# Performance work log

Measured on AMD Instinct MI355X. Metric: run time of the kernel, lower is better.

## Reference

```python
import jax, jax.numpy as jnp
import numpy as np

PATCH = 16       # patch_size
HALF = 8         # patch_size // 2
SEARCH_HALF = 20 # search_size // 2
NCAND = 40       # candidates per axis (stride=1)
WIN = NCAND + PATCH  # 56: search window side
NUM_PATCHES = 256
IMG_RES = 256    # hard-coded in `patch_ids * H // 256`
EPS = 1e-7


def setup_inputs() -> dict:
    key = jax.random.key(0)
    k0, k1, k2, k3, k4 = jax.random.split(key, 5)
    feat0 = jax.random.normal(k0, (1, 3, 256, 256), jnp.float32)
    feat1 = jax.random.normal(k1, (1, 256, 256, 256), jnp.float32)
    feat2 = jax.random.normal(k2, (1, 512, 128, 128), jnp.float32)
    feat3 = jax.random.normal(k3, (1, 1024, 64, 64), jnp.float32)
    # interior location so the 40x40 candidate grid is full (static shape)
    sample_loc = jax.random.randint(k4, (2,), 28, 228, dtype=jnp.int32)
    return {"feat0": feat0, "feat1": feat1, "feat2": feat2,
            "feat3": feat3, "sample_loc": sample_loc}


def _l2norm(x):
    # Normalize(power=2): x / (sqrt(sum(x^2, dim=1)) + 1e-7)
    norm = jnp.sqrt(jnp.sum(x * x, axis=1, keepdims=True))
    return x / (norm + EPS)


def _select_patch_ids(img, sample_loc):
    # brute-force SSD search of 16x16 patches in a 40x40 stride-1 grid
    C = img.shape[1]
    lh, lw = sample_loc[0], sample_loc[1]
    window = jax.lax.dynamic_slice(
        img, (0, 0, lh - SEARCH_HALF - HALF, lw - SEARCH_HALF - HALF),
        (1, C, WIN, WIN))[0]                       # [C,56,56]
    idx = jnp.arange(NCAND)[:, None] + jnp.arange(PATCH)[None, :]  # [40,16]
    # all candidate patches: [C,40,40,16,16]
    patches = window[:, idx[:, None, :, None], idx[None, :, None, :]]
    sample = jax.lax.dynamic_slice(
        img, (0, 0, lh - HALF, lw - HALF), (1, C, PATCH, PATCH))[0]  # [C,16,16]
    diff = patches - sample[:, None, None, :, :]
    dist = jnp.sqrt(jnp.sum(diff * diff, axis=(0, 3, 4)))  # [40,40] L2 distance
    # topk smallest, sorted ascending
    _, top_idx = jax.lax.top_k(-dist.reshape(-1), NUM_PATCHES)
    hs = lh - SEARCH_HALF + jnp.arange(NCAND)
    ws = lw - SEARCH_HALF + jnp.arange(NCAND)
    locs = jnp.stack(jnp.meshgrid(hs, ws, indexing='ij'), axis=-1).reshape(-1, 2)
    return locs[top_idx].astype(jnp.int32)  # [256,2]


def _gather_norm(feat, patch_ids):
    B, C, H, W = feat.shape
    feat_reshape = feat.transpose(0, 2, 3, 1).reshape(B, H * W, C)
    feat_patch_loc = (patch_ids * H) // IMG_RES          # floor_divide
    patch_id = feat_patch_loc[:, 0] * W + feat_patch_loc[:, 1]
    x_sample = feat_reshape[:, patch_id, :].reshape(-1, C)  # [B*256, C]
    return _l2norm(x_sample)


def reference(feat0, feat1, feat2, feat3, sample_loc):
    patch_ids = _select_patch_ids(feat0, sample_loc)
    outs = tuple(_gather_norm(f, patch_ids) for f in (feat0, feat1, feat2, feat3))
    return (*outs, patch_ids)
```

## Files before the change

kernel.cpp:

```cpp
#include <hip/hip_runtime.h>

#define NCAND 40
#define NC2   1600
#define NP    256

__global__ void k_dist(const float* __restrict__ feat0,
                       const int* __restrict__ loc,
                       float* __restrict__ dist) {
    __shared__ float smp[3 * 16 * 16];
    const int lh = loc[0], lw = loc[1];
    for (int t = threadIdx.x; t < 768; t += 256) {
        int c = t >> 8;
        int rem = t & 255;
        int a = rem >> 4;
        int b = rem & 15;
        smp[t] = feat0[c * 65536 + (lh - 8 + a) * 256 + (lw - 8 + b)];
    }
    __syncthreads();

    const int wid  = threadIdx.x >> 6;
    const int lane = threadIdx.x & 63;
    const int cand = blockIdx.x * 4 + wid;
    const int i = cand / NCAND;
    const int j = cand % NCAND;
    const int base_h = lh - 28 + i;
    const int base_w = lw - 28 + j;

    int c = lane >> 4;
    if (c > 2) c = 0;
    const int h = (lane >> 3) & 1;
    const int u = lane & 7;
    const float* fp = feat0 + c * 65536;
    const float* sc = smp + c * 256;

    float r = 0.0f;
#pragma unroll
    for (int k = 0; k < 16; ++k) {
        const int idx = h * 128 + k * 8 + u;
        const int a = idx >> 4;
        const int b = idx & 15;
        float v = fp[(base_h + a) * 256 + base_w + b];
        float d = __fsub_rn(v, sc[idx]);
        float sq = __fmul_rn(d, d);
        r = (k == 0) ? sq : __fadd_rn(r, sq);
    }
    r = __fadd_rn(r, __shfl_xor(r, 1, 64));
    r = __fadd_rn(r, __shfl_xor(r, 2, 64));
    r = __fadd_rn(r, __shfl_xor(r, 4, 64));
    r = __fadd_rn(r, __shfl_xor(r, 8, 64));
    float p1 = __shfl(r, 16, 64);
    float p2 = __shfl(r, 32, 64);
    float tot = __fadd_rn(__fadd_rn(r, p1), p2);
    if (lane == 0) dist[cand] = __fsqrt_rn(tot);
}

__global__ void k_rank(const float* __restrict__ dist,
                       const int* __restrict__ loc,
                       int* __restrict__ hw,
                       float* __restrict__ out_ids) {
    __shared__ float ds[NC2];
    for (int k = threadIdx.x; k < NC2; k += 256) ds[k] = dist[k];
    __syncthreads();

    const int wid  = threadIdx.x >> 6;
    const int lane = threadIdx.x & 63;
    const int t = blockIdx.x * 4 + wid;
    const float dt = ds[t];
    int rank = 0;
#pragma unroll
    for (int m = 0; m < NC2 / 64; ++m) {
        const int k = lane + (m << 6);
        const float dk = ds[k];
        rank += (dk < dt || (dk == dt && k < t)) ? 1 : 0;
    }
    rank += __shfl_xor(rank, 1, 64);
    rank += __shfl_xor(rank, 2, 64);
    rank += __shfl_xor(rank, 4, 64);
    rank += __shfl_xor(rank, 8, 64);
    rank += __shfl_xor(rank, 16, 64);
    rank += __shfl_xor(rank, 32, 64);

    if (lane == 0 && rank < NP) {
        const int lh = loc[0], lw = loc[1];
        const int h = lh - 20 + t / NCAND;
        const int w = lw - 20 + t % NCAND;
        hw[rank * 2]     = h;
        hw[rank * 2 + 1] = w;
        out_ids[rank * 2]     = (float)h;
        out_ids[rank * 2 + 1] = (float)w;
    }
}

__global__ void k_gather(const float* __restrict__ f0,
                         const float* __restrict__ f1,
                         const float* __restrict__ f2,
                         const float* __restrict__ f3,
                         const int* __restrict__ hw,
                         float* __restrict__ out) {
    const int r = blockIdx.x & 255;
    const int f = blockIdx.x >> 8;

    const float* src;
    int C, H;
    long off;
    if (f == 0)      { src = f0; C = 3;    H = 256; off = 0; }
    else if (f == 1) { src = f1; C = 256;  H = 256; off = 768; }
    else if (f == 2) { src = f2; C = 512;  H = 128; off = 768 + 65536; }
    else             { src = f3; C = 1024; H = 64;  off = 768 + 65536 + 131072; }
    const int W = H;

    const int h = hw[r * 2], w = hw[r * 2 + 1];
    const int hh = (h * H) / 256;
    const int ww = (w * H) / 256;
    const long base = (long)hh * W + ww;
    const long HW = (long)H * W;

    float x[4];
    double acc = 0.0;
    int n = 0;
    for (int c = threadIdx.x; c < C; c += 256) {
        float v = src[(long)c * HW + base];
        x[n++] = v;
        acc = fma((double)v, (double)v, acc);
    }

    for (int o = 32; o > 0; o >>= 1) acc += __shfl_down(acc, o, 64);
    __shared__ double red[4];
    const int lane = threadIdx.x & 63;
    const int wid  = threadIdx.x >> 6;
    if (lane == 0) red[wid] = acc;
    __syncthreads();
    const double total = red[0] + red[1] + red[2] + red[3];
    const float scale = (float)(1.0 / (sqrt(total) + 1e-7));

    n = 0;
    for (int c = threadIdx.x; c < C; c += 256) {
        out[off + (long)r * C + c] = x[n++] * scale;
    }
}

extern "C" void kernel_launch(void* const* d_in, const int* in_sizes, int n_in,
                              void* d_out, int out_size, void* d_ws, size_t ws_size,
                              hipStream_t stream) {
    const float* feat0 = (const float*)d_in[0];
    const float* feat1 = (const float*)d_in[1];
    const float* feat2 = (const float*)d_in[2];
    const float* feat3 = (const float*)d_in[3];
    const int*   loc   = (const int*)d_in[4];
    float* out = (float*)d_out;

    float* dist = (float*)d_ws;
    int* hw = (int*)((char*)d_ws + NC2 * sizeof(float));

    float* out_ids = out + 768 + 65536 + 131072 + 262144;

    k_dist<<<NC2 / 4, 256, 0, stream>>>(feat0, loc, dist);
    k_rank<<<NC2 / 4, 256, 0, stream>>>(dist, loc, hw, out_ids);
    k_gather<<<4 * NP, 256, 0, stream>>>(feat0, feat1, feat2, feat3, hw, out);
}
```

Before: 18.74 us.

## Fuse rank and gather kernels so each winning wave gathers its features

Merges the ranking and gather/normalize kernels into one launch. Each wave whose candidate ranks within the top 256 writes the patch id and then gathers and L2-normalizes all four feature maps itself, with fully unrolled templated loops. This removes one kernel launch and the global round-trip through the hw workspace, and replaces the double-precision block reduction with a float wave-level shuffle reduction. In exchange, only 256 of 1600 waves do gather work, so parallelism is low and load is imbalanced, and float accumulation may differ slightly from the double version.

```diff
diff --git a/kernel.cpp b/kernel.cpp
--- a/kernel.cpp
+++ b/kernel.cpp
@@ -54,10 +54,45 @@
     if (lane == 0) dist[cand] = __fsqrt_rn(tot);
 }
 
-__global__ void k_rank(const float* __restrict__ dist,
-                       const int* __restrict__ loc,
-                       int* __restrict__ hw,
-                       float* __restrict__ out_ids) {
+template <int C, int H>
+__device__ __forceinline__ void wave_gather(const float* __restrict__ src,
+                                            long off, int r, int h, int w,
+                                            int lane, float* __restrict__ out) {
+    const int hh = (h * H) / 256;
+    const int ww = (w * H) / 256;
+    const long HW = (long)H * H;
+    const long base = (long)hh * H + ww;
+
+    float x[(C + 63) / 64];
+    float acc = 0.f;
+#pragma unroll
+    for (int m = 0; m < (C + 63) / 64; ++m) {
+        const int c = lane + m * 64;
+        float v = (c < C) ? src[(long)c * HW + base] : 0.f;
+        x[m] = v;
+        acc = fmaf(v, v, acc);
+    }
+    acc += __shfl_xor(acc, 1, 64);
+    acc += __shfl_xor(acc, 2, 64);
+    acc += __shfl_xor(acc, 4, 64);
+    acc += __shfl_xor(acc, 8, 64);
+    acc += __shfl_xor(acc, 16, 64);
+    acc += __shfl_xor(acc, 32, 64);
+    const float scale = 1.0f / (sqrtf(acc) + 1e-7f);
+#pragma unroll
+    for (int m = 0; m < (C + 63) / 64; ++m) {
+        const int c = lane + m * 64;
+        if (c < C) out[off + (long)r * C + c] = x[m] * scale;
+    }
+}
+
+__global__ void k_rankgather(const float* __restrict__ dist,
+                             const int* __restrict__ loc,
+                             const float* __restrict__ feat0,
+                             const float* __restrict__ feat1,
+                             const float* __restrict__ feat2,
+                             const float* __restrict__ feat3,
+                             float* __restrict__ out) {
     __shared__ float ds[NC2];
     for (int k = threadIdx.x; k < NC2; k += 256) ds[k] = dist[k];
     __syncthreads();
@@ -80,62 +115,19 @@
     rank += __shfl_xor(rank, 16, 64);
     rank += __shfl_xor(rank, 32, 64);
 
-    if (lane == 0 && rank < NP) {
+    if (rank < NP) {
         const int lh = loc[0], lw = loc[1];
         const int h = lh - 20 + t / NCAND;
         const int w = lw - 20 + t % NCAND;
-        hw[rank * 2]     = h;
-        hw[rank * 2 + 1] = w;
-        out_ids[rank * 2]     = (float)h;
-        out_ids[rank * 2 + 1] = (float)w;
-    }
-}
-
-__global__ void k_gather(const float* __restrict__ f0,
-                         const float* __restrict__ f1,
-                         const float* __restrict__ f2,
-                         const float* __restrict__ f3,
-                         const int* __restrict__ hw,
-                         float* __restrict__ out) {
-    const int r = blockIdx.x & 255;
-    const int f = blockIdx.x >> 8;
-
-    const float* src;
-    int C, H;
-    long off;
-    if (f == 0)      { src = f0; C = 3;    H = 256; off = 0; }
-    else if (f == 1) { src = f1; C = 256;  H = 256; off = 768; }
-    else if (f == 2) { src = f2; C = 512;  H = 128; off = 768 + 65536; }
-    else             { src = f3; C = 1024; H = 64;  off = 768 + 65536 + 131072; }
-    const int W = H;
-
-    const int h = hw[r * 2], w = hw[r * 2 + 1];
-    const int hh = (h * H) / 256;
-    const int ww = (w * H) / 256;
-    const long base = (long)hh * W + ww;
-    const long HW = (long)H * W;
-
-    float x[4];
-    double acc = 0.0;
-    int n = 0;
-    for (int c = threadIdx.x; c < C; c += 256) {
-        float v = src[(long)c * HW + base];
-        x[n++] = v;
-        acc = fma((double)v, (double)v, acc);
-    }
-
-    for (int o = 32; o > 0; o >>= 1) acc += __shfl_down(acc, o, 64);
-    __shared__ double red[4];
-    const int lane = threadIdx.x & 63;
-    const int wid  = threadIdx.x >> 6;
-    if (lane == 0) red[wid] = acc;
-    __syncthreads();
-    const double total = red[0] + red[1] + red[2] + red[3];
-    const float scale = (float)(1.0 / (sqrt(total) + 1e-7));
-
-    n = 0;
-    for (int c = threadIdx.x; c < C; c += 256) {
-        out[off + (long)r * C + c] = x[n++] * scale;
+        if (lane == 0) {
+            float* out_ids = out + 768 + 65536 + 131072 + 262144;
+            out_ids[rank * 2]     = (float)h;
+            out_ids[rank * 2 + 1] = (float)w;
+        }
+        wave_gather<3,    256>(feat0, 0,                      rank, h, w, lane, out);
+        wave_gather<256,  256>(feat1, 768,                    rank, h, w, lane, out);
+        wave_gather<512,  128>(feat2, 768 + 65536,            rank, h, w, lane, out);
+        wave_gather<1024, 64 >(feat3, 768 + 65536 + 131072,   rank, h, w, lane, out);
     }
 }
 
@@ -150,11 +142,7 @@
     float* out = (float*)d_out;
 
     float* dist = (float*)d_ws;
-    int* hw = (int*)((char*)d_ws + NC2 * sizeof(float));
-
-    float* out_ids = out + 768 + 65536 + 131072 + 262144;
 
     k_dist<<<NC2 / 4, 256, 0, stream>>>(feat0, loc, dist);
-    k_rank<<<NC2 / 4, 256, 0, stream>>>(dist, loc, hw, out_ids);
-    k_gather<<<4 * NP, 256, 0, stream>>>(feat0, feat1, feat2, feat3, hw, out);
+    k_rankgather<<<NC2 / 4, 256, 0, stream>>>(dist, loc, feat0, feat1, feat2, feat3, out);
 }
```

New measurement: 19.80 us. 1.06x slower.
